# Performance work log

Hardware: AMD Instinct MI355X
Metric: run time of the kernel (lower is better)

## Reference

```python
import jax, jax.numpy as jnp
import numpy as np

EPS = 1e-7  # tf.keras.backend.epsilon()
NUM_CAPSULE = 5
DIM_CAPSULE = 5
ROUTINGS = 4


def squash(x, axis=-1):
    s = jnp.sum(x * x, axis=axis, keepdims=True)
    return x / jnp.sqrt(s + EPS)


def setup_inputs() -> dict:
    key = jax.random.key(0)
    k1, k2 = jax.random.split(key)
    B, T, D = 512, 2048, 100
    x = jax.random.normal(k1, (B, T, D), dtype=jnp.float32)
    # glorot_normal for shape (1, 100, 25): std = sqrt(2/(100+25))
    W = jax.random.normal(k2, (1, D, NUM_CAPSULE * DIM_CAPSULE), dtype=jnp.float32) * np.sqrt(2.0 / (D + NUM_CAPSULE * DIM_CAPSULE)).astype(np.float32)
    return {"x": x, "W": W}


def reference(x, W):
    B, T, D = x.shape
    # u_hat: (B, T, N*Dc) -> (B, T, N, Dc) -> (B, N, T, Dc)
    u_hat = jnp.matmul(x, W)  # W broadcasts over batch
    u_hat = u_hat.reshape(B, T, NUM_CAPSULE, DIM_CAPSULE).transpose(0, 2, 1, 3)
    b = jnp.zeros((B, NUM_CAPSULE, T), dtype=x.dtype)
    outputs = None
    for i in range(ROUTINGS):
        # softmax over the num_capsule axis (axis=1 of (B, N, T))
        c = jax.nn.softmax(b, axis=1)
        outputs = squash(jnp.einsum('bnt,bntd->bnd', c, u_hat))
        if i < ROUTINGS - 1:
            b = jnp.einsum('bnd,bntd->bnt', outputs, u_hat)
    return outputs
```

## Files before the change

kernel.cpp:

```cpp
#include <hip/hip_runtime.h>


#define NCAP 5
#define NJ 25
#define NROUT 4
#define TT 2048
#define DD 100
#define TILE 256
#define XSS 101
#define NTH 1024
#define NWAVE 16

__global__ __launch_bounds__(NTH) void caps_fused(
    const float* __restrict__ gx,
    const float* __restrict__ gw,
    float* __restrict__ gout)
{
    __shared__ float xs[TILE * XSS];
    __shared__ float ut[TILE * NJ];
    __shared__ float red[NWAVE * NJ];
    __shared__ float sv[NJ];

    const int tid  = threadIdx.x;
    const int bidx = blockIdx.x;
    const int lane = tid & 63;
    const int wid  = __builtin_amdgcn_readfirstlane(tid >> 6);
    const int ks   = wid / 5;
    const int jg   = wid % 5;
    const int jb   = jg * 5;
    const int k0   = (ks == 0) ? 0  : (ks == 1 ? 34 : 67);
    const int k1   = (ks == 0) ? 34 : (ks == 1 ? 67 : 100);

    const float* xb = gx + (size_t)bidx * (TT * DD);

    float u[2][NJ];

    for (int c = 0; c < 8; ++c) {
        const float* src = xb + c * (TILE * DD);
        #pragma unroll
        for (int s = 0; s < 25; ++s) {
            int i  = tid + s * NTH;
            int rl = i / DD;
            xs[i + rl] = src[i];
        }
        __syncthreads();

        float acc[4][5];
        if (wid < 15) {
            #pragma unroll
            for (int r = 0; r < 4; ++r)
                #pragma unroll
                for (int j = 0; j < 5; ++j) acc[r][j] = 0.f;
            for (int k = k0; k < k1; ++k) {
                float wv[5];
                #pragma unroll
                for (int j = 0; j < 5; ++j) wv[j] = gw[k * NJ + jb + j];
                #pragma unroll
                for (int r = 0; r < 4; ++r) {
                    float xv = xs[(lane + 64 * r) * XSS + k];
                    #pragma unroll
                    for (int j = 0; j < 5; ++j) acc[r][j] += xv * wv[j];
                }
            }
        }

        if (wid < 15 && ks == 0) {
            #pragma unroll
            for (int r = 0; r < 4; ++r)
                #pragma unroll
                for (int j = 0; j < 5; ++j)
                    ut[(lane + 64 * r) * NJ + jb + j] = acc[r][j];
        }
        __syncthreads();
        if (wid < 15 && ks == 1) {
            #pragma unroll
            for (int r = 0; r < 4; ++r)
                #pragma unroll
                for (int j = 0; j < 5; ++j)
                    ut[(lane + 64 * r) * NJ + jb + j] += acc[r][j];
        }
        __syncthreads();
        if (wid < 15 && ks == 2) {
            #pragma unroll
            for (int r = 0; r < 4; ++r)
                #pragma unroll
                for (int j = 0; j < 5; ++j)
                    ut[(lane + 64 * r) * NJ + jb + j] += acc[r][j];
        }
        __syncthreads();

        if ((tid >> 7) == c) {
            int tl = tid & 127;
            #pragma unroll
            for (int r = 0; r < 2; ++r)
                #pragma unroll
                for (int j = 0; j < NJ; ++j)
                    u[r][j] = ut[(2 * tl + r) * NJ + j];
        }
        __syncthreads();
    }

    float bv[2][NCAP];
    #pragma unroll
    for (int r = 0; r < 2; ++r)
        #pragma unroll
        for (int n = 0; n < NCAP; ++n) bv[r][n] = 0.f;

    for (int it = 0; it < NROUT; ++it) {
        float ps[NJ];
        #pragma unroll
        for (int j = 0; j < NJ; ++j) ps[j] = 0.f;

        #pragma unroll
        for (int r = 0; r < 2; ++r) {
            float mx = bv[r][0];
            #pragma unroll
            for (int n = 1; n < NCAP; ++n) mx = fmaxf(mx, bv[r][n]);
            float e[NCAP]; float se = 0.f;
            #pragma unroll
            for (int n = 0; n < NCAP; ++n) { e[n] = expf(bv[r][n] - mx); se += e[n]; }
            float ci = 1.f / se;
            #pragma unroll
            for (int n = 0; n < NCAP; ++n) {
                float cn = e[n] * ci;
                #pragma unroll
                for (int d = 0; d < 5; ++d) ps[n * 5 + d] += cn * u[r][n * 5 + d];
            }
        }

        #pragma unroll
        for (int j = 0; j < NJ; ++j) {
            float v = ps[j];
            #pragma unroll
            for (int m = 1; m < 64; m <<= 1) v += __shfl_xor(v, m, 64);
            ps[j] = v;
        }
        if (lane == 0) {
            #pragma unroll
            for (int j = 0; j < NJ; ++j) red[wid * NJ + j] = ps[j];
        }
        __syncthreads();
        if (tid < NJ) {
            float s = 0.f;
            #pragma unroll
            for (int w = 0; w < NWAVE; ++w) s += red[w * NJ + tid];
            sv[tid] = s;
        }
        __syncthreads();

        if (it < NROUT - 1) {
            float svr[NJ];
            #pragma unroll
            for (int j = 0; j < NJ; ++j) svr[j] = sv[j];
            float nr[NCAP];
            #pragma unroll
            for (int n = 0; n < NCAP; ++n) {
                float ss = 0.f;
                #pragma unroll
                for (int d = 0; d < 5; ++d) ss += svr[n * 5 + d] * svr[n * 5 + d];
                nr[n] = 1.f / sqrtf(ss + 1e-7f);
            }
            #pragma unroll
            for (int r = 0; r < 2; ++r)
                #pragma unroll
                for (int n = 0; n < NCAP; ++n) {
                    float t = 0.f;
                    #pragma unroll
                    for (int d = 0; d < 5; ++d) t += svr[n * 5 + d] * u[r][n * 5 + d];
                    bv[r][n] = nr[n] * t;
                }
        } else {
            if (tid < NJ) {
                int n = tid / 5;
                float ss = 0.f;
                #pragma unroll
                for (int d = 0; d < 5; ++d) ss += sv[n * 5 + d] * sv[n * 5 + d];
                gout[(size_t)bidx * NJ + tid] = sv[tid] * (1.f / sqrtf(ss + 1e-7f));
            }
        }
        __syncthreads();
    }
}

extern "C" void kernel_launch(void* const* d_in, const int* in_sizes, int n_in,
                              void* d_out, int out_size, void* d_ws, size_t ws_size,
                              hipStream_t stream) {
    const float* x = (const float*)d_in[0];
    const float* w = (const float*)d_in[1];
    float* out     = (float*)d_out;
    int B = in_sizes[0] / (TT * DD);
    caps_fused<<<dim3(B), dim3(NTH), 0, stream>>>(x, w, out);
}
```

Measured before the change: 841.7 us.

## Prefetch x tiles into registers and simplify per-row matmul split

Shrinks the x tile to 128 rows with 16 chunks and prefetches the next tile into float4 registers while the current tile is computed, overlapping global loads with the projection. The three-way k-split with serialized shared-memory accumulation is replaced by 640 threads each computing one row's 5 outputs over all 100 k, which removes two barriers per chunk. It also requests 4 waves per SIMD via launch bounds and reads sv directly from shared memory instead of copying it to registers. The costs are register pressure from the prefetch buffers, 384 threads idle during the projection, and longer per-thread k loops.

```diff
diff --git a/kernel.cpp b/kernel.cpp
--- a/kernel.cpp
+++ b/kernel.cpp
@@ -6,12 +6,13 @@
 #define NROUT 4
 #define TT 2048
 #define DD 100
-#define TILE 256
+#define TILE 128
+#define NCHUNK 16
 #define XSS 101
 #define NTH 1024
 #define NWAVE 16
 
-__global__ __launch_bounds__(NTH) void caps_fused(
+__global__ __launch_bounds__(NTH, 4) void caps_fused(
     const float* __restrict__ gx,
     const float* __restrict__ gw,
     float* __restrict__ gout)
@@ -25,79 +26,73 @@
     const int bidx = blockIdx.x;
     const int lane = tid & 63;
     const int wid  = __builtin_amdgcn_readfirstlane(tid >> 6);
-    const int ks   = wid / 5;
-    const int jg   = wid % 5;
-    const int jb   = jg * 5;
-    const int k0   = (ks == 0) ? 0  : (ks == 1 ? 34 : 67);
-    const int k1   = (ks == 0) ? 34 : (ks == 1 ? 67 : 100);
+    const int jg5  = __builtin_amdgcn_readfirstlane(tid >> 7) * 5;
+    const int rloc = tid & 127;
 
     const float* xb = gx + (size_t)bidx * (TT * DD);
 
     float u[2][NJ];
+    float4 st0, st1, st2, st3;
 
-    for (int c = 0; c < 8; ++c) {
-        const float* src = xb + c * (TILE * DD);
-        #pragma unroll
-        for (int s = 0; s < 25; ++s) {
-            int i  = tid + s * NTH;
-            int rl = i / DD;
-            xs[i + rl] = src[i];
-        }
+    {
+        const float4* s4 = (const float4*)xb;
+        st0 = s4[tid]; st1 = s4[tid + 1024]; st2 = s4[tid + 2048];
+        if (tid < 128) st3 = s4[tid + 3072];
+    }
+
+    for (int c = 0; c < NCHUNK; ++c) {
         __syncthreads();
 
-        float acc[4][5];
-        if (wid < 15) {
-            #pragma unroll
-            for (int r = 0; r < 4; ++r)
-                #pragma unroll
-                for (int j = 0; j < 5; ++j) acc[r][j] = 0.f;
-            for (int k = k0; k < k1; ++k) {
-                float wv[5];
-                #pragma unroll
-                for (int j = 0; j < 5; ++j) wv[j] = gw[k * NJ + jb + j];
-                #pragma unroll
-                for (int r = 0; r < 4; ++r) {
-                    float xv = xs[(lane + 64 * r) * XSS + k];
-                    #pragma unroll
-                    for (int j = 0; j < 5; ++j) acc[r][j] += xv * wv[j];
-                }
+        {
+            int e, rl, b;
+            e = 4 * tid;          rl = e / DD; b = e + rl;
+            xs[b] = st0.x; xs[b+1] = st0.y; xs[b+2] = st0.z; xs[b+3] = st0.w;
+            e = 4 * (tid + 1024); rl = e / DD; b = e + rl;
+            xs[b] = st1.x; xs[b+1] = st1.y; xs[b+2] = st1.z; xs[b+3] = st1.w;
+            e = 4 * (tid + 2048); rl = e / DD; b = e + rl;
+            xs[b] = st2.x; xs[b+1] = st2.y; xs[b+2] = st2.z; xs[b+3] = st2.w;
+            if (tid < 128) {
+                e = 4 * (tid + 3072); rl = e / DD; b = e + rl;
+                xs[b] = st3.x; xs[b+1] = st3.y; xs[b+2] = st3.z; xs[b+3] = st3.w;
             }
         }
-
-        if (wid < 15 && ks == 0) {
-            #pragma unroll
-            for (int r = 0; r < 4; ++r)
-                #pragma unroll
-                for (int j = 0; j < 5; ++j)
-                    ut[(lane + 64 * r) * NJ + jb + j] = acc[r][j];
-        }
-        __syncthreads();
-        if (wid < 15 && ks == 1) {
-            #pragma unroll
-            for (int r = 0; r < 4; ++r)
-                #pragma unroll
-                for (int j = 0; j < 5; ++j)
-                    ut[(lane + 64 * r) * NJ + jb + j] += acc[r][j];
-        }
-        __syncthreads();
-        if (wid < 15 && ks == 2) {
-            #pragma unroll
-            for (int r = 0; r < 4; ++r)
-                #pragma unroll
-                for (int j = 0; j < 5; ++j)
-                    ut[(lane + 64 * r) * NJ + jb + j] += acc[r][j];
-        }
-        __syncthreads();
-
-        if ((tid >> 7) == c) {
-            int tl = tid & 127;
+        if (c > 0 && wid == c - 1) {
             #pragma unroll
             for (int r = 0; r < 2; ++r)
                 #pragma unroll
                 for (int j = 0; j < NJ; ++j)
-                    u[r][j] = ut[(2 * tl + r) * NJ + j];
+                    u[r][j] = ut[(2 * lane + r) * NJ + j];
         }
         __syncthreads();
+
+        if (c < NCHUNK - 1) {
+            const float4* s4 = (const float4*)(xb + (c + 1) * (TILE * DD));
+            st0 = s4[tid]; st1 = s4[tid + 1024]; st2 = s4[tid + 2048];
+            if (tid < 128) st3 = s4[tid + 3072];
+        }
+
+        if (tid < 640) {
+            float a0 = 0.f, a1 = 0.f, a2 = 0.f, a3 = 0.f, a4 = 0.f;
+            const float* xrow = xs + rloc * XSS;
+            const float* wp   = gw + jg5;
+            #pragma unroll 4
+            for (int k = 0; k < DD; ++k) {
+                float xv = xrow[k];
+                const float* w5 = wp + k * NJ;
+                a0 += xv * w5[0]; a1 += xv * w5[1]; a2 += xv * w5[2];
+                a3 += xv * w5[3]; a4 += xv * w5[4];
+            }
+            int ro = rloc * NJ + jg5;
+            ut[ro+0] = a0; ut[ro+1] = a1; ut[ro+2] = a2; ut[ro+3] = a3; ut[ro+4] = a4;
+        }
+    }
+    __syncthreads();
+    if (wid == NCHUNK - 1) {
+        #pragma unroll
+        for (int r = 0; r < 2; ++r)
+            #pragma unroll
+            for (int j = 0; j < NJ; ++j)
+                u[r][j] = ut[(2 * lane + r) * NJ + j];
     }
 
     float bv[2][NCAP];
@@ -149,15 +144,12 @@
         __syncthreads();
 
         if (it < NROUT - 1) {
-            float svr[NJ];
-            #pragma unroll
-            for (int j = 0; j < NJ; ++j) svr[j] = sv[j];
             float nr[NCAP];
             #pragma unroll
             for (int n = 0; n < NCAP; ++n) {
                 float ss = 0.f;
                 #pragma unroll
-                for (int d = 0; d < 5; ++d) ss += svr[n * 5 + d] * svr[n * 5 + d];
+                for (int d = 0; d < 5; ++d) ss += sv[n * 5 + d] * sv[n * 5 + d];
                 nr[n] = 1.f / sqrtf(ss + 1e-7f);
             }
             #pragma unroll
@@ -166,7 +158,7 @@
                 for (int n = 0; n < NCAP; ++n) {
                     float t = 0.f;
                     #pragma unroll
-                    for (int d = 0; d < 5; ++d) t += svr[n * 5 + d] * u[r][n * 5 + d];
+                    for (int d = 0; d < 5; ++d) t += sv[n * 5 + d] * u[r][n * 5 + d];
                     bv[r][n] = nr[n] * t;
                 }
         } else {
```

New measurement: 745.3 us. 1.13x faster.
